# Performance work log

Measured on AMD Instinct MI355X. Metric: run time of the kernel, lower is better.

## Reference

```python
import jax, jax.numpy as jnp
import numpy as np

B, S, H, D = 8, 1024, 16, 64  # batch, seq, heads, d_heads; hidden = H*D = 1024

def setup_inputs() -> dict:
    key = jax.random.key(0)
    ks = jax.random.split(key, 7)
    sc = 1.0 / np.sqrt(D)
    return {
        "sequences": jax.random.normal(ks[0], (B, S, H * D), dtype=jnp.float32),
        "Wq": jax.random.normal(ks[1], (H, D, D), dtype=jnp.float32) * sc,
        "bq": jax.random.normal(ks[2], (H, D), dtype=jnp.float32) * 0.01,
        "Wk": jax.random.normal(ks[3], (H, D, D), dtype=jnp.float32) * sc,
        "bk": jax.random.normal(ks[4], (H, D), dtype=jnp.float32) * 0.01,
        "Wv": jax.random.normal(ks[5], (H, D, D), dtype=jnp.float32) * sc,
        "bv": jax.random.normal(ks[6], (H, D), dtype=jnp.float32) * 0.01,
    }

def reference(sequences, Wq, bq, Wk, bk, Wv, bv):
    # sequences: [B, S, H*D] -> [B, S, H, D] (head h uses slice h*D:(h+1)*D)
    x = sequences.reshape(B, S, H, D)
    # per-head Linear: y = x @ W.T + b  (torch convention)
    q = jnp.einsum("bshd,hed->bshe", x, Wq) + bq
    k = jnp.einsum("bshd,hed->bshe", x, Wk) + bk
    v = jnp.einsum("bshd,hed->bshe", x, Wv) + bv
    scores = jnp.einsum("bqhd,bkhd->bhqk", q, k) / jnp.sqrt(jnp.float32(D))
    attn = jax.nn.softmax(scores, axis=-1)
    out = jnp.einsum("bhqk,bkhd->bqhd", attn, v)  # [B, S, H, D]
    return out.reshape(B, S, H * D)  # hstack over heads == reshape
```

## Files before the change

kernel.cpp:

```cpp
#include <hip/hip_runtime.h>
#include <hip/hip_bf16.h>


typedef __attribute__((ext_vector_type(8))) short short8;
typedef __attribute__((ext_vector_type(4))) float f32x4;
typedef __attribute__((ext_vector_type(16))) float f32x16;
typedef __attribute__((ext_vector_type(4))) unsigned short u16x4;
typedef __attribute__((ext_vector_type(2))) unsigned int u32x2;
typedef __attribute__((ext_vector_type(4))) unsigned int u32x4;

#define MFMA16 __builtin_amdgcn_mfma_f32_16x16x32_bf16
#define MFMA32 __builtin_amdgcn_mfma_f32_32x32x16_bf16

#define QSCALE 0.1803368801111204f

__device__ __forceinline__ unsigned cvt_pk(float lo, float hi) {
  unsigned r;
  asm("v_cvt_pk_bf16_f32 %0, %1, %2" : "=v"(r) : "v"(lo), "v"(hi));
  return r;
}
__device__ __forceinline__ void pl32_swap(unsigned &a, unsigned &b) {
  asm("v_permlane32_swap_b32 %0, %1" : "+v"(a), "+v"(b));
}
__device__ __forceinline__ u32x2 pk4(const f32x4 v) {
  return (u32x2){cvt_pk(v[0], v[1]), cvt_pk(v[2], v[3])};
}

__global__ __launch_bounds__(256) void qkv_proj_kernel(
    const float* __restrict__ x,
    const float* __restrict__ Wq, const float* __restrict__ bq,
    const float* __restrict__ Wk, const float* __restrict__ bk,
    const float* __restrict__ Wv, const float* __restrict__ bv,
    unsigned short* __restrict__ qt_ws,
    unsigned short* __restrict__ kv_ws)
{
  __shared__ unsigned short x_lds[64][72];
  __shared__ unsigned short w_lds[3][64][72];

  const int h    = blockIdx.x & 15;
  const int tb   = blockIdx.x >> 4;
  const int tid  = threadIdx.x;
  const int lane = tid & 63;
  const int wv   = tid >> 6;
  const int g    = lane >> 4;
  const int cc   = lane & 15;

  {
    const int i  = tid >> 2;
    const int q4 = tid & 3;
    const float* xs  = x  + (size_t)(tb * 64 + i) * 1024 + h * 64 + q4 * 16;
    const float* wsq = Wq + (size_t)h * 4096 + i * 64 + q4 * 16;
    const float* wsk = Wk + (size_t)h * 4096 + i * 64 + q4 * 16;
    const float* wsv = Wv + (size_t)h * 4096 + i * 64 + q4 * 16;
#pragma unroll
    for (int it = 0; it < 4; ++it) {
      const int c = q4 * 16 + it * 4;
      *(u32x2*)&x_lds[i][c]    = pk4(*(const f32x4*)(xs  + it * 4));
      *(u32x2*)&w_lds[0][i][c] = pk4(*(const f32x4*)(wsq + it * 4));
      *(u32x2*)&w_lds[1][i][c] = pk4(*(const f32x4*)(wsk + it * 4));
      *(u32x2*)&w_lds[2][i][c] = pk4(*(const f32x4*)(wsv + it * 4));
    }
  }
  __syncthreads();

  f32x4 aq[4], ak[4], av[4];
#pragma unroll
  for (int f = 0; f < 4; ++f) {
    aq[f] = (f32x4){0.f, 0.f, 0.f, 0.f};
    ak[f] = (f32x4){0.f, 0.f, 0.f, 0.f};
    av[f] = (f32x4){0.f, 0.f, 0.f, 0.f};
  }

  const int arow = wv * 16 + cc;
  const int kc   = g * 8;
#pragma unroll
  for (int kk = 0; kk < 2; ++kk) {
    short8 a = *(const short8*)&x_lds[arow][kk * 32 + kc];
#pragma unroll
    for (int f = 0; f < 4; ++f) {
      const int br = f * 16 + cc;
      aq[f] = MFMA16(a, *(const short8*)&w_lds[0][br][kk * 32 + kc], aq[f], 0, 0, 0);
      ak[f] = MFMA16(a, *(const short8*)&w_lds[1][br][kk * 32 + kc], ak[f], 0, 0, 0);
      av[f] = MFMA16(a, *(const short8*)&w_lds[2][br][kk * 32 + kc], av[f], 0, 0, 0);
    }
  }

  const int b   = tb >> 4;
  const int s0  = (tb & 15) << 6;
  const int tk0 = wv * 16 + g * 4;
  const size_t qbase = ((size_t)(b * 16 + h)) << 16;
  unsigned short* kvt = kv_ws + (size_t)(b * 16 + h) * 131072 + (size_t)(tb & 15) * 8192;

  __syncthreads();
  unsigned short* Ak = &w_lds[0][0][0];
  unsigned short* Av = &x_lds[0][0];

#pragma unroll
  for (int f = 0; f < 4; ++f) {
    const int e = f * 16 + cc;
    const float bqs = bq[h * 64 + e] * QSCALE;
    const float bkv = bk[h * 64 + e];
    const float bvv = bv[h * 64 + e];
    f32x4 vq, vk, vv;
#pragma unroll
    for (int r = 0; r < 4; ++r) {
      vq[r] = fmaf(aq[f][r], QSCALE, bqs);
      vk[r] = ak[f][r] + bkv;
      vv[r] = av[f][r] + bvv;
    }
    *(u32x2*)&qt_ws[qbase + ((size_t)e << 10) + s0 + tk0] = pk4(vq);
    *(u32x2*)&Av[e * 72 + tk0] = pk4(vv);
    u32x2 pkk = pk4(vk);
    Ak[(tk0 + 0) * 72 + e] = (unsigned short)pkk[0];
    Ak[(tk0 + 1) * 72 + e] = (unsigned short)(pkk[0] >> 16);
    Ak[(tk0 + 2) * 72 + e] = (unsigned short)pkk[1];
    Ak[(tk0 + 3) * 72 + e] = (unsigned short)(pkk[1] >> 16);
  }
  __syncthreads();

#pragma unroll
  for (int half = 0; half < 2; ++half) {
    const int c   = tid + half * 256;
    const int oct = c >> 6;
    const int r2  = c & 63;
    const int slot = (oct >> 1) * 128 + (r2 >> 5) * 64 + (oct & 1) * 32 + (r2 & 31);
    short8 kcnk = *(const short8*)&Ak[r2 * 72 + oct * 8];
    *(short8*)&kvt[slot * 8] = kcnk;
    short8 vcnk = *(const short8*)&Av[r2 * 72 + oct * 8];
    *(short8*)&kvt[4096 + slot * 8] = vcnk;
  }
}

__global__ __launch_bounds__(512, 4) void attn_kernel(
    const unsigned short* __restrict__ qt_ws,
    const unsigned short* __restrict__ kv_ws,
    float* __restrict__ out)
{
  __shared__ __align__(16) char lds[32768];

  const int logical = (blockIdx.x & 7) * 64 + (blockIdx.x >> 3);
  const int qt = logical & 3;
  const int bh = logical >> 2;
  const int b  = bh >> 4;
  const int h  = bh & 15;
  const size_t qbase = (size_t)bh << 16;
  const unsigned short* kvb = kv_ws + (size_t)bh * 131072;

  const int tid = threadIdx.x;
  const int w   = tid >> 6;
  const int l   = tid & 63;
  const int hi  = l >> 5;
  const int cc  = l & 31;

  short8 qf[4];
  {
    const unsigned short* qp0 =
        qt_ws + qbase + (size_t)(hi * 8) * 1024 + (qt * 256 + w * 32 + cc);
#pragma unroll
    for (int c = 0; c < 4; ++c) {
      short8 t;
#pragma unroll
      for (int j = 0; j < 8; ++j)
        t[j] = (short)qp0[(size_t)(c * 16 + j) << 10];
      qf[c] = t;
    }
  }

  const unsigned short* sgp = kvb + tid * 8;
  char* wbp = lds + tid * 16;

  short8 st[2];
#pragma unroll
  for (int j = 0; j < 2; ++j) st[j] = *(const short8*)(sgp + j * 4096);
#pragma unroll
  for (int j = 0; j < 2; ++j) *(short8*)(wbp + j * 8192) = st[j];
#pragma unroll
  for (int j = 0; j < 2; ++j) st[j] = *(const short8*)(sgp + 8192 + j * 4096);
  __syncthreads();

  f32x16 ot0 = {}; f32x16 ot1 = {};
  float lsum = 0.f;

  for (int kv = 0; kv < 16; ++kv) {
    if (kv < 15) {
      char* d = wbp + ((kv + 1) & 1) * 16384;
#pragma unroll
      for (int j = 0; j < 2; ++j) *(short8*)(d + j * 8192) = st[j];
      if (kv < 14) {
        const unsigned short* s = sgp + (size_t)(kv + 2) * 8192;
#pragma unroll
        for (int j = 0; j < 2; ++j) st[j] = *(const short8*)(s + j * 4096);
      }
    }
    const char* kb_ = lds + (kv & 1) * 16384;
    const char* vb_ = kb_ + 8192;

    f32x16 s0 = {}; f32x16 s1 = {};
    __builtin_amdgcn_s_setprio(1);
#pragma unroll
    for (int c = 0; c < 4; ++c) {
      s0 = MFMA32(*(const short8*)(kb_ + (c * 128 + l) * 16),      qf[c], s0, 0, 0, 0);
      s1 = MFMA32(*(const short8*)(kb_ + (c * 128 + 64 + l) * 16), qf[c], s1, 0, 0, 0);
    }
    __builtin_amdgcn_s_setprio(0);

    float ps0 = 0.f, ps1 = 0.f;
#pragma unroll
    for (int i = 0; i < 16; ++i) { s0[i] = __builtin_amdgcn_exp2f(s0[i]); ps0 += s0[i]; }
#pragma unroll
    for (int i = 0; i < 16; ++i) { s1[i] = __builtin_amdgcn_exp2f(s1[i]); ps1 += s1[i]; }
    lsum += ps0 + ps1;

#pragma unroll
    for (int kb = 0; kb < 2; ++kb) {
      const f32x16& p = kb ? s1 : s0;
      unsigned d0 = cvt_pk(p[0],  p[1]);
      unsigned d2 = cvt_pk(p[4],  p[5]);
      pl32_swap(d0, d2);
      unsigned d1 = cvt_pk(p[2],  p[3]);
      unsigned d3 = cvt_pk(p[6],  p[7]);
      pl32_swap(d1, d3);
      u32x4 pa0u = {d0, d1, d2, d3};
      unsigned e0 = cvt_pk(p[8],  p[9]);
      unsigned e2 = cvt_pk(p[12], p[13]);
      pl32_swap(e0, e2);
      unsigned e1 = cvt_pk(p[10], p[11]);
      unsigned e3 = cvt_pk(p[14], p[15]);
      pl32_swap(e1, e3);
      u32x4 pa1u = {e0, e1, e2, e3};
      short8 pa0 = __builtin_bit_cast(short8, pa0u);
      short8 pa1 = __builtin_bit_cast(short8, pa1u);

      const int c20 = kb * 2, c21 = kb * 2 + 1;
      __builtin_amdgcn_s_setprio(1);
      ot0 = MFMA32(*(const short8*)(vb_ + (c20 * 128 + l) * 16),      pa0, ot0, 0, 0, 0);
      ot1 = MFMA32(*(const short8*)(vb_ + (c20 * 128 + 64 + l) * 16), pa0, ot1, 0, 0, 0);
      ot0 = MFMA32(*(const short8*)(vb_ + (c21 * 128 + l) * 16),      pa1, ot0, 0, 0, 0);
      ot1 = MFMA32(*(const short8*)(vb_ + (c21 * 128 + 64 + l) * 16), pa1, ot1, 0, 0, 0);
      __builtin_amdgcn_s_setprio(0);
    }
    __syncthreads();
  }

  const float lt  = lsum + __shfl_xor(lsum, 32, 64);
  const float inv = 1.0f / lt;
  const int s_row = qt * 256 + w * 32 + cc;
  float* op = out + ((size_t)(b * 1024 + s_row) << 10) + h * 64;
#pragma unroll
  for (int rg = 0; rg < 4; ++rg) {
    const int d0 = 8 * rg + 4 * hi;
    f32x4 v0, v1;
#pragma unroll
    for (int j = 0; j < 4; ++j) {
      v0[j] = ot0[rg * 4 + j] * inv;
      v1[j] = ot1[rg * 4 + j] * inv;
    }
    *(f32x4*)(op + d0)      = v0;
    *(f32x4*)(op + 32 + d0) = v1;
  }
}

extern "C" void kernel_launch(void* const* d_in, const int* in_sizes, int n_in,
                              void* d_out, int out_size, void* d_ws, size_t ws_size,
                              hipStream_t stream) {
  const float* x  = (const float*)d_in[0];
  const float* Wq = (const float*)d_in[1];
  const float* bq = (const float*)d_in[2];
  const float* Wk = (const float*)d_in[3];
  const float* bk = (const float*)d_in[4];
  const float* Wv = (const float*)d_in[5];
  const float* bv = (const float*)d_in[6];
  float* out = (float*)d_out;

  unsigned short* qt_ws = (unsigned short*)d_ws;
  unsigned short* kv_ws = qt_ws + (size_t)8388608;

  qkv_proj_kernel<<<2048, 256, 0, stream>>>(x, Wq, bq, Wk, bk, Wv, bv,
                                            qt_ws, kv_ws);
  attn_kernel<<<512, 512, 0, stream>>>(qt_ws, kv_ws, out);
}
```

Measured before the change: 71.10 us.

## Software-pipeline QK scores one tile ahead with triple-buffered LDS

Attention now computes the QK^T scores for the next KV tile before running softmax and PV on the current one. It moves from double to triple LDS buffering with a prefetch distance of three tiles, and replaces __syncthreads with a manual lgkmcnt wait plus barrier. The goal is to overlap MFMA score work with exp and convert work, and to hide global-load latency. In exchange, LDS grows to 48KB and the occupancy hint drops from 4 to 2, which can reduce latency hiding across waves.

```diff
diff --git a/kernel.cpp b/kernel.cpp
--- a/kernel.cpp
+++ b/kernel.cpp
@@ -24,6 +24,10 @@
 }
 __device__ __forceinline__ u32x2 pk4(const f32x4 v) {
   return (u32x2){cvt_pk(v[0], v[1]), cvt_pk(v[2], v[3])};
+}
+__device__ __forceinline__ void lds_barrier() {
+  asm volatile("s_waitcnt lgkmcnt(0)" ::: "memory");
+  __builtin_amdgcn_s_barrier();
 }
 
 __global__ __launch_bounds__(256) void qkv_proj_kernel(
@@ -131,12 +135,12 @@
   }
 }
 
-__global__ __launch_bounds__(512, 4) void attn_kernel(
+__global__ __launch_bounds__(512, 2) void attn_kernel(
     const unsigned short* __restrict__ qt_ws,
     const unsigned short* __restrict__ kv_ws,
     float* __restrict__ out)
 {
-  __shared__ __align__(16) char lds[32768];
+  __shared__ __align__(16) char lds[49152];
 
   const int logical = (blockIdx.x & 7) * 64 + (blockIdx.x >> 3);
   const int qt = logical & 3;
@@ -169,51 +173,62 @@
   const unsigned short* sgp = kvb + tid * 8;
   char* wbp = lds + tid * 16;
 
-  short8 st[2];
-#pragma unroll
-  for (int j = 0; j < 2; ++j) st[j] = *(const short8*)(sgp + j * 4096);
-#pragma unroll
-  for (int j = 0; j < 2; ++j) *(short8*)(wbp + j * 8192) = st[j];
-#pragma unroll
-  for (int j = 0; j < 2; ++j) st[j] = *(const short8*)(sgp + 8192 + j * 4096);
-  __syncthreads();
+  short8 st[2][2];
+#pragma unroll
+  for (int j = 0; j < 2; ++j) st[0][j] = *(const short8*)(sgp + j * 4096);
+#pragma unroll
+  for (int j = 0; j < 2; ++j) *(short8*)(wbp + j * 8192) = st[0][j];
+#pragma unroll
+  for (int j = 0; j < 2; ++j) st[0][j] = *(const short8*)(sgp + 8192 + j * 4096);
+#pragma unroll
+  for (int j = 0; j < 2; ++j) *(short8*)(wbp + 16384 + j * 8192) = st[0][j];
+#pragma unroll
+  for (int j = 0; j < 2; ++j) st[0][j] = *(const short8*)(sgp + 16384 + j * 4096);
+  lds_barrier();
 
   f32x16 ot0 = {}; f32x16 ot1 = {};
   float lsum = 0.f;
-
+  f32x16 S0[2], S1[2];
+
+  {
+    const char* kb_ = lds;
+    f32x16 a = {}; f32x16 b2 = {};
+#pragma unroll
+    for (int c = 0; c < 4; ++c) {
+      a  = MFMA32(*(const short8*)(kb_ + (c * 128 + l) * 16),      qf[c], a,  0, 0, 0);
+      b2 = MFMA32(*(const short8*)(kb_ + (c * 128 + 64 + l) * 16), qf[c], b2, 0, 0, 0);
+    }
+    S0[0] = a; S1[0] = b2;
+  }
+
+#pragma unroll
   for (int kv = 0; kv < 16; ++kv) {
+    const int cA = kv & 1, cB = cA ^ 1;
+
     if (kv < 15) {
-      char* d = wbp + ((kv + 1) & 1) * 16384;
-#pragma unroll
-      for (int j = 0; j < 2; ++j) *(short8*)(d + j * 8192) = st[j];
-      if (kv < 14) {
-        const unsigned short* s = sgp + (size_t)(kv + 2) * 8192;
-#pragma unroll
-        for (int j = 0; j < 2; ++j) st[j] = *(const short8*)(s + j * 4096);
+      const char* kb_ = lds + ((kv + 1) % 3) * 16384;
+      f32x16 a = {}; f32x16 b2 = {};
+      __builtin_amdgcn_s_setprio(1);
+#pragma unroll
+      for (int c = 0; c < 4; ++c) {
+        a  = MFMA32(*(const short8*)(kb_ + (c * 128 + l) * 16),      qf[c], a,  0, 0, 0);
+        b2 = MFMA32(*(const short8*)(kb_ + (c * 128 + 64 + l) * 16), qf[c], b2, 0, 0, 0);
       }
-    }
-    const char* kb_ = lds + (kv & 1) * 16384;
-    const char* vb_ = kb_ + 8192;
-
-    f32x16 s0 = {}; f32x16 s1 = {};
-    __builtin_amdgcn_s_setprio(1);
-#pragma unroll
-    for (int c = 0; c < 4; ++c) {
-      s0 = MFMA32(*(const short8*)(kb_ + (c * 128 + l) * 16),      qf[c], s0, 0, 0, 0);
-      s1 = MFMA32(*(const short8*)(kb_ + (c * 128 + 64 + l) * 16), qf[c], s1, 0, 0, 0);
-    }
-    __builtin_amdgcn_s_setprio(0);
+      __builtin_amdgcn_s_setprio(0);
+      S0[cB] = a; S1[cB] = b2;
+    }
 
     float ps0 = 0.f, ps1 = 0.f;
 #pragma unroll
-    for (int i = 0; i < 16; ++i) { s0[i] = __builtin_amdgcn_exp2f(s0[i]); ps0 += s0[i]; }
-#pragma unroll
-    for (int i = 0; i < 16; ++i) { s1[i] = __builtin_amdgcn_exp2f(s1[i]); ps1 += s1[i]; }
+    for (int i = 0; i < 16; ++i) { S0[cA][i] = __builtin_amdgcn_exp2f(S0[cA][i]); ps0 += S0[cA][i]; }
+#pragma unroll
+    for (int i = 0; i < 16; ++i) { S1[cA][i] = __builtin_amdgcn_exp2f(S1[cA][i]); ps1 += S1[cA][i]; }
     lsum += ps0 + ps1;
 
+    const char* vb_ = lds + (kv % 3) * 16384 + 8192;
 #pragma unroll
     for (int kb = 0; kb < 2; ++kb) {
-      const f32x16& p = kb ? s1 : s0;
+      const f32x16& p = kb ? S1[cA] : S0[cA];
       unsigned d0 = cvt_pk(p[0],  p[1]);
       unsigned d2 = cvt_pk(p[4],  p[5]);
       pl32_swap(d0, d2);
@@ -239,7 +254,18 @@
       ot1 = MFMA32(*(const short8*)(vb_ + (c21 * 128 + 64 + l) * 16), pa1, ot1, 0, 0, 0);
       __builtin_amdgcn_s_setprio(0);
     }
-    __syncthreads();
+
+    if (kv < 14) {
+      char* d = wbp + ((kv + 2) % 3) * 16384;
+#pragma unroll
+      for (int j = 0; j < 2; ++j) *(short8*)(d + j * 8192) = st[kv & 1][j];
+    }
+    if (kv < 13) {
+      const unsigned short* s = sgp + (size_t)(kv + 3) * 8192;
+#pragma unroll
+      for (int j = 0; j < 2; ++j) st[(kv + 1) & 1][j] = *(const short8*)(s + j * 4096);
+    }
+    if (kv < 15) lds_barrier();
   }
 
   const float lt  = lsum + __shfl_xor(lsum, 32, 64);
```

Result: slower. 73.01 us (+2.7%).

## Pre-pack weights into MFMA fragment layout and load projection operands directly to registers

Applied to the files above, without the earlier changes.

Adds a small kernel that converts Wq/Wk/Wv to bf16 in MFMA B-fragment order, so the projection kernel loads fragments straight from global memory. The x operand is also read directly into registers instead of being staged through LDS. This removes the first barrier and most of the LDS traffic from the projection kernel and lets it run at 4 blocks per CU. The attention kernel's __syncthreads is replaced with an lgkmcnt wait plus s_barrier, which drops the wait on outstanding global loads so prefetch can overlap the barrier. The cost is one extra kernel launch and redundant global weight reads across the 2048 blocks, which should mostly hit in cache.

```diff
diff --git a/kernel.cpp b/kernel.cpp
--- a/kernel.cpp
+++ b/kernel.cpp
@@ -5,7 +5,6 @@
 typedef __attribute__((ext_vector_type(8))) short short8;
 typedef __attribute__((ext_vector_type(4))) float f32x4;
 typedef __attribute__((ext_vector_type(16))) float f32x16;
-typedef __attribute__((ext_vector_type(4))) unsigned short u16x4;
 typedef __attribute__((ext_vector_type(2))) unsigned int u32x2;
 typedef __attribute__((ext_vector_type(4))) unsigned int u32x4;
 
@@ -25,17 +24,42 @@
 __device__ __forceinline__ u32x2 pk4(const f32x4 v) {
   return (u32x2){cvt_pk(v[0], v[1]), cvt_pk(v[2], v[3])};
 }
-
-__global__ __launch_bounds__(256) void qkv_proj_kernel(
+__device__ __forceinline__ void lds_barrier() {
+  asm volatile("s_waitcnt lgkmcnt(0)" ::: "memory");
+  __builtin_amdgcn_s_barrier();
+}
+
+__global__ __launch_bounds__(256) void wconv_kernel(
+    const float* __restrict__ Wq, const float* __restrict__ Wk,
+    const float* __restrict__ Wv, unsigned short* __restrict__ wf)
+{
+  const int gid = blockIdx.x * 256 + threadIdx.x;
+  const int F   = gid >> 6;
+  const int l   = gid & 63;
+  const int kk  = F & 1;
+  const int f   = (F >> 1) & 3;
+  const int mh  = F >> 3;
+  const int h   = mh / 3;
+  const int mat = mh - h * 3;
+  const float* W = (mat == 0) ? Wq : ((mat == 1) ? Wk : Wv);
+  const float* src = W + h * 4096 + (f * 16 + (l & 15)) * 64 + kk * 32 + (l >> 4) * 8;
+  f32x4 v0 = *(const f32x4*)src;
+  f32x4 v1 = *(const f32x4*)(src + 4);
+  u32x4 d = {cvt_pk(v0[0], v0[1]), cvt_pk(v0[2], v0[3]),
+             cvt_pk(v1[0], v1[1]), cvt_pk(v1[2], v1[3])};
+  *(u32x4*)(wf + (size_t)F * 512 + l * 8) = d;
+}
+
+__global__ __launch_bounds__(256, 4) void qkv_proj_kernel(
     const float* __restrict__ x,
-    const float* __restrict__ Wq, const float* __restrict__ bq,
-    const float* __restrict__ Wk, const float* __restrict__ bk,
-    const float* __restrict__ Wv, const float* __restrict__ bv,
+    const float* __restrict__ bq, const float* __restrict__ bk,
+    const float* __restrict__ bv,
+    const unsigned short* __restrict__ wf,
     unsigned short* __restrict__ qt_ws,
     unsigned short* __restrict__ kv_ws)
 {
-  __shared__ unsigned short x_lds[64][72];
-  __shared__ unsigned short w_lds[3][64][72];
+  __shared__ unsigned short Ak[64][72];
+  __shared__ unsigned short Av[64][72];
 
   const int h    = blockIdx.x & 15;
   const int tb   = blockIdx.x >> 4;
@@ -45,55 +69,42 @@
   const int g    = lane >> 4;
   const int cc   = lane & 15;
 
+  short8 a[2];
   {
-    const int i  = tid >> 2;
-    const int q4 = tid & 3;
-    const float* xs  = x  + (size_t)(tb * 64 + i) * 1024 + h * 64 + q4 * 16;
-    const float* wsq = Wq + (size_t)h * 4096 + i * 64 + q4 * 16;
-    const float* wsk = Wk + (size_t)h * 4096 + i * 64 + q4 * 16;
-    const float* wsv = Wv + (size_t)h * 4096 + i * 64 + q4 * 16;
-#pragma unroll
-    for (int it = 0; it < 4; ++it) {
-      const int c = q4 * 16 + it * 4;
-      *(u32x2*)&x_lds[i][c]    = pk4(*(const f32x4*)(xs  + it * 4));
-      *(u32x2*)&w_lds[0][i][c] = pk4(*(const f32x4*)(wsq + it * 4));
-      *(u32x2*)&w_lds[1][i][c] = pk4(*(const f32x4*)(wsk + it * 4));
-      *(u32x2*)&w_lds[2][i][c] = pk4(*(const f32x4*)(wsv + it * 4));
-    }
-  }
-  __syncthreads();
-
-  f32x4 aq[4], ak[4], av[4];
-#pragma unroll
-  for (int f = 0; f < 4; ++f) {
-    aq[f] = (f32x4){0.f, 0.f, 0.f, 0.f};
-    ak[f] = (f32x4){0.f, 0.f, 0.f, 0.f};
-    av[f] = (f32x4){0.f, 0.f, 0.f, 0.f};
-  }
-
-  const int arow = wv * 16 + cc;
-  const int kc   = g * 8;
-#pragma unroll
-  for (int kk = 0; kk < 2; ++kk) {
-    short8 a = *(const short8*)&x_lds[arow][kk * 32 + kc];
-#pragma unroll
-    for (int f = 0; f < 4; ++f) {
-      const int br = f * 16 + cc;
-      aq[f] = MFMA16(a, *(const short8*)&w_lds[0][br][kk * 32 + kc], aq[f], 0, 0, 0);
-      ak[f] = MFMA16(a, *(const short8*)&w_lds[1][br][kk * 32 + kc], ak[f], 0, 0, 0);
-      av[f] = MFMA16(a, *(const short8*)&w_lds[2][br][kk * 32 + kc], av[f], 0, 0, 0);
-    }
-  }
+    const float* xs = x + (size_t)(tb * 64 + wv * 16 + cc) * 1024 + h * 64 + g * 8;
+#pragma unroll
+    for (int kk = 0; kk < 2; ++kk) {
+      f32x4 v0 = *(const f32x4*)(xs + kk * 32);
+      f32x4 v1 = *(const f32x4*)(xs + kk * 32 + 4);
+      u32x4 d = {cvt_pk(v0[0], v0[1]), cvt_pk(v0[2], v0[3]),
+                 cvt_pk(v1[0], v1[1]), cvt_pk(v1[2], v1[3])};
+      a[kk] = __builtin_bit_cast(short8, d);
+    }
+  }
+
+  f32x4 acc[3][4];
+#pragma unroll
+  for (int m = 0; m < 3; ++m)
+#pragma unroll
+    for (int f = 0; f < 4; ++f) acc[m][f] = (f32x4){0.f, 0.f, 0.f, 0.f};
+
+  const unsigned short* wfh = wf + (size_t)(h * 3) * 8 * 512 + lane * 8;
+#pragma unroll
+  for (int kk = 0; kk < 2; ++kk)
+#pragma unroll
+    for (int f = 0; f < 4; ++f)
+#pragma unroll
+      for (int m = 0; m < 3; ++m) {
+        short8 bfrag = *(const short8*)(wfh + (m * 8 + f * 2 + kk) * 512);
+        acc[m][f] = MFMA16(a[kk], bfrag, acc[m][f], 0, 0, 0);
+      }
 
   const int b   = tb >> 4;
   const int s0  = (tb & 15) << 6;
   const int tk0 = wv * 16 + g * 4;
   const size_t qbase = ((size_t)(b * 16 + h)) << 16;
-  unsigned short* kvt = kv_ws + (size_t)(b * 16 + h) * 131072 + (size_t)(tb & 15) * 8192;
-
-  __syncthreads();
-  unsigned short* Ak = &w_lds[0][0][0];
-  unsigned short* Av = &x_lds[0][0];
+  unsigned short* kvt = kv_ws + (size_t)(b * 16 + h) * 131072
+                              + (size_t)(tb & 15) * 8192;
 
 #pragma unroll
   for (int f = 0; f < 4; ++f) {
@@ -101,20 +112,21 @@
     const float bqs = bq[h * 64 + e] * QSCALE;
     const float bkv = bk[h * 64 + e];
     const float bvv = bv[h * 64 + e];
-    f32x4 vq, vk, vv;
-#pragma unroll
-    for (int r = 0; r < 4; ++r) {
-      vq[r] = fmaf(aq[f][r], QSCALE, bqs);
-      vk[r] = ak[f][r] + bkv;
-      vv[r] = av[f][r] + bvv;
-    }
+    f32x4 vq;
+#pragma unroll
+    for (int r = 0; r < 4; ++r) vq[r] = fmaf(acc[0][f][r], QSCALE, bqs);
     *(u32x2*)&qt_ws[qbase + ((size_t)e << 10) + s0 + tk0] = pk4(vq);
-    *(u32x2*)&Av[e * 72 + tk0] = pk4(vv);
-    u32x2 pkk = pk4(vk);
-    Ak[(tk0 + 0) * 72 + e] = (unsigned short)pkk[0];
-    Ak[(tk0 + 1) * 72 + e] = (unsigned short)(pkk[0] >> 16);
-    Ak[(tk0 + 2) * 72 + e] = (unsigned short)pkk[1];
-    Ak[(tk0 + 3) * 72 + e] = (unsigned short)(pkk[1] >> 16);
+    u32x2 pkk;
+    pkk[0] = cvt_pk(acc[1][f][0] + bkv, acc[1][f][1] + bkv);
+    pkk[1] = cvt_pk(acc[1][f][2] + bkv, acc[1][f][3] + bkv);
+    Ak[tk0 + 0][e] = (unsigned short)pkk[0];
+    Ak[tk0 + 1][e] = (unsigned short)(pkk[0] >> 16);
+    Ak[tk0 + 2][e] = (unsigned short)pkk[1];
+    Ak[tk0 + 3][e] = (unsigned short)(pkk[1] >> 16);
+    f32x4 vv;
+#pragma unroll
+    for (int r = 0; r < 4; ++r) vv[r] = acc[2][f][r] + bvv;
+    *(u32x2*)&Av[e][tk0] = pk4(vv);
   }
   __syncthreads();
 
@@ -124,9 +136,9 @@
     const int oct = c >> 6;
     const int r2  = c & 63;
     const int slot = (oct >> 1) * 128 + (r2 >> 5) * 64 + (oct & 1) * 32 + (r2 & 31);
-    short8 kcnk = *(const short8*)&Ak[r2 * 72 + oct * 8];
+    short8 kcnk = *(const short8*)&Ak[r2][oct * 8];
     *(short8*)&kvt[slot * 8] = kcnk;
-    short8 vcnk = *(const short8*)&Av[r2 * 72 + oct * 8];
+    short8 vcnk = *(const short8*)&Av[r2][oct * 8];
     *(short8*)&kvt[4096 + slot * 8] = vcnk;
   }
 }
@@ -176,7 +188,7 @@
   for (int j = 0; j < 2; ++j) *(short8*)(wbp + j * 8192) = st[j];
 #pragma unroll
   for (int j = 0; j < 2; ++j) st[j] = *(const short8*)(sgp + 8192 + j * 4096);
-  __syncthreads();
+  lds_barrier();
 
   f32x16 ot0 = {}; f32x16 ot1 = {};
   float lsum = 0.f;
@@ -239,7 +251,7 @@
       ot1 = MFMA32(*(const short8*)(vb_ + (c21 * 128 + 64 + l) * 16), pa1, ot1, 0, 0, 0);
       __builtin_amdgcn_s_setprio(0);
     }
-    __syncthreads();
+    lds_barrier();
   }
 
   const float lt  = lsum + __shfl_xor(lsum, 32, 64);
@@ -274,8 +286,10 @@
 
   unsigned short* qt_ws = (unsigned short*)d_ws;
   unsigned short* kv_ws = qt_ws + (size_t)8388608;
-
-  qkv_proj_kernel<<<2048, 256, 0, stream>>>(x, Wq, bq, Wk, bk, Wv, bv,
+  unsigned short* wf_ws = kv_ws + (size_t)16777216;
+
+  wconv_kernel<<<96, 256, 0, stream>>>(Wq, Wk, Wv, wf_ws);
+  qkv_proj_kernel<<<2048, 256, 0, stream>>>(x, bq, bk, bv, wf_ws,
                                             qt_ws, kv_ws);
   attn_kernel<<<512, 512, 0, stream>>>(qt_ws, kv_ws, out);
 }
```

Measured after the change: 76.02 us. +6.9%, slower.

## Fuse Q projection into attention kernel and drop Q workspace round trip

Applied to the files above, without the earlier changes.

Q is no longer computed in the projection kernel and stored to a transposed bf16 workspace. Each attention wave now loads its x rows and Wq slices in fp32, converts them to bf16, runs 32x32 MFMAs to form Q, adds bias and scale, and repacks the accumulators into MFMA B-operand fragments. This removes the Q write and the strided 2-byte gather reads of the old path, and shrinks the projection kernel's LDS and work. The cost is redundant Wq loads in every attention block and extra work before the KV loop starts. Block barriers are also replaced with an explicit lgkmcnt wait plus s_barrier.

```diff
diff --git a/kernel.cpp b/kernel.cpp
--- a/kernel.cpp
+++ b/kernel.cpp
@@ -5,7 +5,6 @@
 typedef __attribute__((ext_vector_type(8))) short short8;
 typedef __attribute__((ext_vector_type(4))) float f32x4;
 typedef __attribute__((ext_vector_type(16))) float f32x16;
-typedef __attribute__((ext_vector_type(4))) unsigned short u16x4;
 typedef __attribute__((ext_vector_type(2))) unsigned int u32x2;
 typedef __attribute__((ext_vector_type(4))) unsigned int u32x4;
 
@@ -25,17 +24,44 @@
 __device__ __forceinline__ u32x2 pk4(const f32x4 v) {
   return (u32x2){cvt_pk(v[0], v[1]), cvt_pk(v[2], v[3])};
 }
-
-__global__ __launch_bounds__(256) void qkv_proj_kernel(
+__device__ __forceinline__ short8 ld8bf(const float* p) {
+  f32x4 v0 = *(const f32x4*)p;
+  f32x4 v1 = *(const f32x4*)(p + 4);
+  u32x4 d = {cvt_pk(v0[0], v0[1]), cvt_pk(v0[2], v0[3]),
+             cvt_pk(v1[0], v1[1]), cvt_pk(v1[2], v1[3])};
+  return __builtin_bit_cast(short8, d);
+}
+__device__ __forceinline__ void pack_cd(const f32x16& p, short8& lo, short8& hi8) {
+  unsigned d0 = cvt_pk(p[0],  p[1]);
+  unsigned d2 = cvt_pk(p[4],  p[5]);
+  pl32_swap(d0, d2);
+  unsigned d1 = cvt_pk(p[2],  p[3]);
+  unsigned d3 = cvt_pk(p[6],  p[7]);
+  pl32_swap(d1, d3);
+  u32x4 a = {d0, d1, d2, d3};
+  unsigned e0 = cvt_pk(p[8],  p[9]);
+  unsigned e2 = cvt_pk(p[12], p[13]);
+  pl32_swap(e0, e2);
+  unsigned e1 = cvt_pk(p[10], p[11]);
+  unsigned e3 = cvt_pk(p[14], p[15]);
+  pl32_swap(e1, e3);
+  u32x4 b = {e0, e1, e2, e3};
+  lo  = __builtin_bit_cast(short8, a);
+  hi8 = __builtin_bit_cast(short8, b);
+}
+__device__ __forceinline__ void lds_barrier() {
+  asm volatile("s_waitcnt lgkmcnt(0)" ::: "memory");
+  __builtin_amdgcn_s_barrier();
+}
+
+__global__ __launch_bounds__(256) void kv_proj_kernel(
     const float* __restrict__ x,
-    const float* __restrict__ Wq, const float* __restrict__ bq,
     const float* __restrict__ Wk, const float* __restrict__ bk,
     const float* __restrict__ Wv, const float* __restrict__ bv,
-    unsigned short* __restrict__ qt_ws,
     unsigned short* __restrict__ kv_ws)
 {
   __shared__ unsigned short x_lds[64][72];
-  __shared__ unsigned short w_lds[3][64][72];
+  __shared__ unsigned short w_lds[2][64][72];
 
   const int h    = blockIdx.x & 15;
   const int tb   = blockIdx.x >> 4;
@@ -49,24 +75,21 @@
     const int i  = tid >> 2;
     const int q4 = tid & 3;
     const float* xs  = x  + (size_t)(tb * 64 + i) * 1024 + h * 64 + q4 * 16;
-    const float* wsq = Wq + (size_t)h * 4096 + i * 64 + q4 * 16;
     const float* wsk = Wk + (size_t)h * 4096 + i * 64 + q4 * 16;
     const float* wsv = Wv + (size_t)h * 4096 + i * 64 + q4 * 16;
 #pragma unroll
     for (int it = 0; it < 4; ++it) {
       const int c = q4 * 16 + it * 4;
       *(u32x2*)&x_lds[i][c]    = pk4(*(const f32x4*)(xs  + it * 4));
-      *(u32x2*)&w_lds[0][i][c] = pk4(*(const f32x4*)(wsq + it * 4));
-      *(u32x2*)&w_lds[1][i][c] = pk4(*(const f32x4*)(wsk + it * 4));
-      *(u32x2*)&w_lds[2][i][c] = pk4(*(const f32x4*)(wsv + it * 4));
+      *(u32x2*)&w_lds[0][i][c] = pk4(*(const f32x4*)(wsk + it * 4));
+      *(u32x2*)&w_lds[1][i][c] = pk4(*(const f32x4*)(wsv + it * 4));
     }
   }
   __syncthreads();
 
-  f32x4 aq[4], ak[4], av[4];
+  f32x4 ak[4], av[4];
 #pragma unroll
   for (int f = 0; f < 4; ++f) {
-    aq[f] = (f32x4){0.f, 0.f, 0.f, 0.f};
     ak[f] = (f32x4){0.f, 0.f, 0.f, 0.f};
     av[f] = (f32x4){0.f, 0.f, 0.f, 0.f};
   }
@@ -79,17 +102,15 @@
 #pragma unroll
     for (int f = 0; f < 4; ++f) {
       const int br = f * 16 + cc;
-      aq[f] = MFMA16(a, *(const short8*)&w_lds[0][br][kk * 32 + kc], aq[f], 0, 0, 0);
-      ak[f] = MFMA16(a, *(const short8*)&w_lds[1][br][kk * 32 + kc], ak[f], 0, 0, 0);
-      av[f] = MFMA16(a, *(const short8*)&w_lds[2][br][kk * 32 + kc], av[f], 0, 0, 0);
+      ak[f] = MFMA16(a, *(const short8*)&w_lds[0][br][kk * 32 + kc], ak[f], 0, 0, 0);
+      av[f] = MFMA16(a, *(const short8*)&w_lds[1][br][kk * 32 + kc], av[f], 0, 0, 0);
     }
   }
 
   const int b   = tb >> 4;
-  const int s0  = (tb & 15) << 6;
   const int tk0 = wv * 16 + g * 4;
-  const size_t qbase = ((size_t)(b * 16 + h)) << 16;
-  unsigned short* kvt = kv_ws + (size_t)(b * 16 + h) * 131072 + (size_t)(tb & 15) * 8192;
+  unsigned short* kvt = kv_ws + (size_t)(b * 16 + h) * 131072
+                              + (size_t)(tb & 15) * 8192;
 
   __syncthreads();
   unsigned short* Ak = &w_lds[0][0][0];
@@ -98,23 +119,19 @@
 #pragma unroll
   for (int f = 0; f < 4; ++f) {
     const int e = f * 16 + cc;
-    const float bqs = bq[h * 64 + e] * QSCALE;
     const float bkv = bk[h * 64 + e];
     const float bvv = bv[h * 64 + e];
-    f32x4 vq, vk, vv;
-#pragma unroll
-    for (int r = 0; r < 4; ++r) {
-      vq[r] = fmaf(aq[f][r], QSCALE, bqs);
-      vk[r] = ak[f][r] + bkv;
-      vv[r] = av[f][r] + bvv;
-    }
-    *(u32x2*)&qt_ws[qbase + ((size_t)e << 10) + s0 + tk0] = pk4(vq);
-    *(u32x2*)&Av[e * 72 + tk0] = pk4(vv);
-    u32x2 pkk = pk4(vk);
+    u32x2 pkk;
+    pkk[0] = cvt_pk(ak[f][0] + bkv, ak[f][1] + bkv);
+    pkk[1] = cvt_pk(ak[f][2] + bkv, ak[f][3] + bkv);
     Ak[(tk0 + 0) * 72 + e] = (unsigned short)pkk[0];
     Ak[(tk0 + 1) * 72 + e] = (unsigned short)(pkk[0] >> 16);
     Ak[(tk0 + 2) * 72 + e] = (unsigned short)pkk[1];
     Ak[(tk0 + 3) * 72 + e] = (unsigned short)(pkk[1] >> 16);
+    f32x4 vv;
+#pragma unroll
+    for (int r = 0; r < 4; ++r) vv[r] = av[f][r] + bvv;
+    *(u32x2*)&Av[e * 72 + tk0] = pk4(vv);
   }
   __syncthreads();
 
@@ -132,7 +149,8 @@
 }
 
 __global__ __launch_bounds__(512, 4) void attn_kernel(
-    const unsigned short* __restrict__ qt_ws,
+    const float* __restrict__ x,
+    const float* __restrict__ Wq, const float* __restrict__ bq,
     const unsigned short* __restrict__ kv_ws,
     float* __restrict__ out)
 {
@@ -143,7 +161,6 @@
   const int bh = logical >> 2;
   const int b  = bh >> 4;
   const int h  = bh & 15;
-  const size_t qbase = (size_t)bh << 16;
   const unsigned short* kvb = kv_ws + (size_t)bh * 131072;
 
   const int tid = threadIdx.x;
@@ -152,31 +169,41 @@
   const int hi  = l >> 5;
   const int cc  = l & 31;
 
+  const unsigned short* sgp = kvb + tid * 8;
+  char* wbp = lds + tid * 16;
+
+  short8 st[2];
+#pragma unroll
+  for (int j = 0; j < 2; ++j) st[j] = *(const short8*)(sgp + j * 4096);
+
   short8 qf[4];
   {
-    const unsigned short* qp0 =
-        qt_ws + qbase + (size_t)(hi * 8) * 1024 + (qt * 256 + w * 32 + cc);
+    const int tok = qt * 256 + w * 32 + cc;
+    const float* xs  = x  + ((size_t)(b * 1024 + tok)) * 1024 + h * 64 + hi * 8;
+    const float* wlo = Wq + h * 4096 + cc * 64 + hi * 8;
+    const float* whi = wlo + 2048;
+    f32x16 qa0 = {}; f32x16 qa1 = {};
 #pragma unroll
     for (int c = 0; c < 4; ++c) {
-      short8 t;
-#pragma unroll
-      for (int j = 0; j < 8; ++j)
-        t[j] = (short)qp0[(size_t)(c * 16 + j) << 10];
-      qf[c] = t;
-    }
-  }
-
-  const unsigned short* sgp = kvb + tid * 8;
-  char* wbp = lds + tid * 16;
-
-  short8 st[2];
-#pragma unroll
-  for (int j = 0; j < 2; ++j) st[j] = *(const short8*)(sgp + j * 4096);
+      short8 xf = ld8bf(xs + c * 16);
+      qa0 = MFMA32(ld8bf(wlo + c * 16), xf, qa0, 0, 0, 0);
+      qa1 = MFMA32(ld8bf(whi + c * 16), xf, qa1, 0, 0, 0);
+    }
+#pragma unroll
+    for (int r = 0; r < 16; ++r) {
+      const int e = (r & 3) + 8 * (r >> 2) + 4 * hi;
+      qa0[r] = (qa0[r] + bq[h * 64 + e]) * QSCALE;
+      qa1[r] = (qa1[r] + bq[h * 64 + 32 + e]) * QSCALE;
+    }
+    pack_cd(qa0, qf[0], qf[1]);
+    pack_cd(qa1, qf[2], qf[3]);
+  }
+
 #pragma unroll
   for (int j = 0; j < 2; ++j) *(short8*)(wbp + j * 8192) = st[j];
 #pragma unroll
   for (int j = 0; j < 2; ++j) st[j] = *(const short8*)(sgp + 8192 + j * 4096);
-  __syncthreads();
+  lds_barrier();
 
   f32x16 ot0 = {}; f32x16 ot1 = {};
   float lsum = 0.f;
@@ -213,23 +240,8 @@
 
 #pragma unroll
     for (int kb = 0; kb < 2; ++kb) {
-      const f32x16& p = kb ? s1 : s0;
-      unsigned d0 = cvt_pk(p[0],  p[1]);
-      unsigned d2 = cvt_pk(p[4],  p[5]);
-      pl32_swap(d0, d2);
-      unsigned d1 = cvt_pk(p[2],  p[3]);
-      unsigned d3 = cvt_pk(p[6],  p[7]);
-      pl32_swap(d1, d3);
-      u32x4 pa0u = {d0, d1, d2, d3};
-      unsigned e0 = cvt_pk(p[8],  p[9]);
-      unsigned e2 = cvt_pk(p[12], p[13]);
-      pl32_swap(e0, e2);
-      unsigned e1 = cvt_pk(p[10], p[11]);
-      unsigned e3 = cvt_pk(p[14], p[15]);
-      pl32_swap(e1, e3);
-      u32x4 pa1u = {e0, e1, e2, e3};
-      short8 pa0 = __builtin_bit_cast(short8, pa0u);
-      short8 pa1 = __builtin_bit_cast(short8, pa1u);
+      short8 pa0, pa1;
+      pack_cd(kb ? s1 : s0, pa0, pa1);
 
       const int c20 = kb * 2, c21 = kb * 2 + 1;
       __builtin_amdgcn_s_setprio(1);
@@ -239,7 +251,7 @@
       ot1 = MFMA32(*(const short8*)(vb_ + (c21 * 128 + 64 + l) * 16), pa1, ot1, 0, 0, 0);
       __builtin_amdgcn_s_setprio(0);
     }
-    __syncthreads();
+    lds_barrier();
   }
 
   const float lt  = lsum + __shfl_xor(lsum, 32, 64);
@@ -272,10 +284,8 @@
   const float* bv = (const float*)d_in[6];
   float* out = (float*)d_out;
 
-  unsigned short* qt_ws = (unsigned short*)d_ws;
-  unsigned short* kv_ws = qt_ws + (size_t)8388608;
-
-  qkv_proj_kernel<<<2048, 256, 0, stream>>>(x, Wq, bq, Wk, bk, Wv, bv,
-                                            qt_ws, kv_ws);
-  attn_kernel<<<512, 512, 0, stream>>>(qt_ws, kv_ws, out);
-}
+  unsigned short* kv_ws = (unsigned short*)d_ws;
+
+  kv_proj_kernel<<<2048, 256, 0, stream>>>(x, Wk, bk, Wv, bv, kv_ws);
+  attn_kernel<<<512, 512, 0, stream>>>(x, Wq, bq, kv_ws, out);
+}
```

After: 73.33 us. 3.1% more time.
